# Performance work log

Hardware: AMD Instinct MI355X
Metric: run time of the kernel (lower is better)

## Reference

```python
import jax, jax.numpy as jnp
import numpy as np

B, T, D, F = 4, 1024, 256, 128  # input_dim=D, feature_dim=F, cat_size=1+F


def prelu(x, a):
    # torch.nn.PReLU with a single shared parameter (default init 0.25)
    return jnp.where(x >= 0, x, a * x)


def setup_inputs() -> dict:
    key = jax.random.key(0)
    ks = jax.random.split(key, 10)
    cat = 1 + F
    s1 = 1.0 / np.sqrt(cat)
    s2 = 1.0 / np.sqrt(F)
    return {
        "input": jax.random.normal(ks[0], (B, T, D), jnp.float32),
        "feature": jax.random.normal(ks[1], (B, T, F), jnp.float32),
        "slider": jax.random.uniform(ks[2], (B, T, 1), jnp.float32),
        "W1": jax.random.uniform(ks[3], (F, cat), jnp.float32, -s1, s1),
        "b1": jax.random.uniform(ks[4], (F,), jnp.float32, -s1, s1),
        "a1": jnp.float32(0.25),
        "W2": jax.random.uniform(ks[5], (F, F), jnp.float32, -s2, s2),
        "b2": jax.random.uniform(ks[6], (F,), jnp.float32, -s2, s2),
        "a2": jnp.float32(0.25),
        "Wp": jax.random.uniform(ks[7], (2, cat), jnp.float32, -s1, s1),
        "bp": jax.random.uniform(ks[8], (2,), jnp.float32, -s1, s1),
    }


def reference(input, feature, slider, W1, b1, a1, W2, b2, a2, Wp, bp):
    # input: (B,T,D) -> (B,T,D,1); feature broadcast over D: (B,T,1,F)
    inp = input[..., None]                       # (B,T,D,1)
    feat = feature[..., None, :]                 # (B,T,1,F)
    feat = jnp.broadcast_to(feat, (B, T, D, F))  # repeat across input_dim
    x = jnp.concatenate((inp, feat), axis=-1)    # (B,T,D,1+F)
    # tmlp: Linear -> PReLU -> Linear -> PReLU
    h = prelu(jnp.einsum('btdc,fc->btdf', x, W1) + b1, a1)  # (B,T,D,F)
    h = prelu(jnp.einsum('btdf,gf->btdg', h, W2) + b2, a2)  # (B,T,D,F)
    y = jnp.concatenate((h, inp), axis=-1)       # (B,T,D,1+F)
    p = jnp.einsum('btdc,oc->btdo', y, Wp) + bp  # (B,T,D,2)
    g = p[..., 0:1] * jax.nn.sigmoid(p[..., 1:2])  # GLU(dim=-1) -> (B,T,D,1)
    return (inp * (1.0 + g)).squeeze(-1)         # (B,T,D)
```

## Files before the change

### kernel.cpp

```cpp
#include <hip/hip_runtime.h>
#include <hip/hip_bf16.h>

#define BT 4096
#define DD 256
#define CAT 129

typedef __attribute__((ext_vector_type(8))) __bf16 bf16x8;
typedef __attribute__((ext_vector_type(4))) float f32x4;

static __device__ __forceinline__ unsigned short f2bf(float x) {
    __bf16 b = (__bf16)x;
    return __builtin_bit_cast(unsigned short, b);
}
static __device__ __forceinline__ __bf16 tobf(float x) { return (__bf16)x; }

__global__ void __launch_bounds__(256) k_cvt(
    const float* __restrict__ W1, const float* __restrict__ W2,
    unsigned short* __restrict__ w2bf, unsigned short* __restrict__ w1bf,
    float* __restrict__ w10f)
{
    const int t = threadIdx.x, b = blockIdx.x;
    if (b < 8) {
        #pragma unroll
        for (int i = 0; i < 8; ++i) {
            int idx = b * 2048 + i * 256 + t;
            int g = idx >> 7;
            w2bf[idx ^ ((g & 7) << 3)] = f2bf(W2[idx]);
        }
    } else {
        int q = b - 8;
        #pragma unroll
        for (int i = 0; i < 8; ++i) {
            int idx = q * 2048 + i * 256 + t;
            int f = idx >> 7, c = idx & 127;
            w1bf[idx ^ ((f & 7) << 3)] = f2bf(W1[f * CAT + 1 + c]);
        }
        if (q == 0 && t < 128) w10f[t] = W1[t * CAT];
    }
}

__global__ void __launch_bounds__(256) k_prep2(
    const float* __restrict__ feature, const unsigned short* __restrict__ w1bf,
    const float* __restrict__ b1p, float* __restrict__ v1g)
{
    __shared__ __align__(16) unsigned short fS[2048];
    const int t = threadIdx.x;
    const int r0 = blockIdx.x * 16;

    {
        int e = t * 8;
        int r = e >> 7, c = e & 127;
        const float4* src = (const float4*)(feature + (size_t)(r0 + r) * 128 + c);
        float4 x0 = src[0], x1 = src[1];
        bf16x8 hv;
        hv[0]=tobf(x0.x); hv[1]=tobf(x0.y); hv[2]=tobf(x0.z); hv[3]=tobf(x0.w);
        hv[4]=tobf(x1.x); hv[5]=tobf(x1.y); hv[6]=tobf(x1.z); hv[7]=tobf(x1.w);
        *(bf16x8*)&fS[e ^ ((r & 7) << 3)] = hv;
    }
    __syncthreads();

    const int lane = t & 63, wv = t >> 6;
    const int l15 = lane & 15, l4 = lane >> 4;

    bf16x8 bfr[2][4];
    float4 b1v[2];
    #pragma unroll
    for (int nt = 0; nt < 2; ++nt) {
        const int f0 = wv * 32 + nt * 16;
        b1v[nt] = *(const float4*)(b1p + f0 + l4 * 4);
        #pragma unroll
        for (int kc = 0; kc < 4; ++kc) {
            int f = f0 + l15, c = kc * 32 + l4 * 8;
            bfr[nt][kc] = *(const bf16x8*)&w1bf[(f * 128 + c) ^ ((f & 7) << 3)];
        }
    }

    const f32x4 fz = {0.f, 0.f, 0.f, 0.f};
    f32x4 acc[2] = {fz, fz};
    #pragma unroll
    for (int kc = 0; kc < 4; ++kc) {
        bf16x8 afr;
        {
            int r = l15, c = kc * 32 + l4 * 8;
            afr = *(const bf16x8*)&fS[(r * 128 + c) ^ ((r & 7) << 3)];
        }
        #pragma unroll
        for (int nt = 0; nt < 2; ++nt)
            acc[nt] = __builtin_amdgcn_mfma_f32_16x16x32_bf16(
                bfr[nt][kc], afr, acc[nt], 0, 0, 0);
    }

    #pragma unroll
    for (int nt = 0; nt < 2; ++nt) {
        float4 o;
        o.x = acc[nt][0] + ((const float*)&b1v[nt])[0];
        o.y = acc[nt][1] + ((const float*)&b1v[nt])[1];
        o.z = acc[nt][2] + ((const float*)&b1v[nt])[2];
        o.w = acc[nt][3] + ((const float*)&b1v[nt])[3];
        *(float4*)(v1g + (size_t)(r0 + l15) * 128 + wv * 32 + nt * 16 + l4 * 4) = o;
    }
}

__global__ void __launch_bounds__(512, 4) k_main(
    const float* __restrict__ inp, const float* __restrict__ b2p,
    const float* __restrict__ Wp, const float* __restrict__ bpp,
    const float* __restrict__ a1p, const float* __restrict__ a2p,
    const float* __restrict__ v1g, const unsigned short* __restrict__ w2bf,
    const float* __restrict__ w10f, float* __restrict__ out)
{
    __shared__ __align__(16) unsigned short h1s[8192];
    __shared__ float v1s[8][20];
    __shared__ float w10s[8][20];
    __shared__ float inps[256];
    __shared__ float b2s[128], wpas[128], wpbs[128];
    __shared__ float2 prs[2][4][64];

    const int tid  = threadIdx.x;
    const int lane = tid & 63, wv = tid >> 6;
    const int rg   = wv >> 2, cg = wv & 3;
    const int l15  = lane & 15, l4 = lane >> 4;
    const int bt   = blockIdx.x;

    const float* inpRow = inp + (size_t)bt * DD;
    const float* v1row  = v1g + (size_t)bt * 128;

    if (tid < 256)      inps[tid] = inpRow[tid];
    else if (tid < 384) b2s[tid - 256] = b2p[tid - 256];
    else                wpas[tid - 384] = Wp[tid - 384];
    if (tid < 128)      wpbs[tid] = Wp[CAT + tid];
    else if (tid < 256) { int f = tid - 128; v1s[f >> 4][f & 15]  = v1row[f]; }
    else if (tid < 384) { int f = tid - 256; w10s[f >> 4][f & 15] = w10f[f]; }

    bf16x8 bfr[2][4];
    #pragma unroll
    for (int nt = 0; nt < 2; ++nt) {
        const int g = cg * 32 + nt * 16 + l15;
        #pragma unroll
        for (int kc = 0; kc < 4; ++kc) {
            const int f = kc * 32 + l4 * 8;
            bfr[nt][kc] = *(const bf16x8*)&w2bf[(g * 128 + f) ^ ((g & 7) << 3)];
        }
    }

    const float a1   = a1p[0], a2v = a2p[0];
    const float wpi0 = Wp[128], wpi1 = Wp[CAT + 128];
    const float bp0  = bpp[0],  bp1  = bpp[1];
    __syncthreads();

    const int lr = tid >> 3;
    const int fg = tid & 7;
    const f32x4 fz = {0.f, 0.f, 0.f, 0.f};

    for (int qt = 0; qt < 4; ++qt) {
        float2* prsC = &prs[qt & 1][0][0];

        {
            const float s = inps[qt * 64 + lr];
            #pragma unroll
            for (int f8 = 0; f8 < 2; ++f8) {
                const float4 va0 = *(const float4*)&v1s[fg][f8 * 8];
                const float4 va1 = *(const float4*)&v1s[fg][f8 * 8 + 4];
                const float4 wa0 = *(const float4*)&w10s[fg][f8 * 8];
                const float4 wa1 = *(const float4*)&w10s[fg][f8 * 8 + 4];
                const float va[8] = {va0.x, va0.y, va0.z, va0.w,
                                     va1.x, va1.y, va1.z, va1.w};
                const float wa[8] = {wa0.x, wa0.y, wa0.z, wa0.w,
                                     wa1.x, wa1.y, wa1.z, wa1.w};
                bf16x8 hv;
                #pragma unroll
                for (int j = 0; j < 8; ++j) {
                    float h = fmaf(wa[j], s, va[j]);
                    h = fmaxf(h, 0.f) + a1 * fminf(h, 0.f);
                    hv[j] = (__bf16)h;
                }
                const int idx = (lr * 128 + fg * 16 + f8 * 8) ^ ((lr & 7) << 3);
                *(bf16x8*)&h1s[idx] = hv;
            }
        }
        __syncthreads();

        f32x4 acc[2][2] = {{fz, fz}, {fz, fz}};
        #pragma unroll
        for (int kc = 0; kc < 4; ++kc) {
            bf16x8 afr[2];
            #pragma unroll
            for (int rt = 0; rt < 2; ++rt) {
                const int r = rg * 32 + rt * 16 + l15;
                const int f = kc * 32 + l4 * 8;
                afr[rt] = *(const bf16x8*)&h1s[(r * 128 + f) ^ ((r & 7) << 3)];
            }
            #pragma unroll
            for (int nt = 0; nt < 2; ++nt)
                #pragma unroll
                for (int rt = 0; rt < 2; ++rt)
                    acc[nt][rt] = __builtin_amdgcn_mfma_f32_16x16x32_bf16(
                        bfr[nt][kc], afr[rt], acc[nt][rt], 0, 0, 0);
        }

        float4 b2q[2], wq0[2], wq1[2];
        #pragma unroll
        for (int nt = 0; nt < 2; ++nt) {
            b2q[nt] = *(const float4*)&b2s[cg * 32 + nt * 16 + l4 * 4];
            wq0[nt] = *(const float4*)&wpas[cg * 32 + nt * 16 + l4 * 4];
            wq1[nt] = *(const float4*)&wpbs[cg * 32 + nt * 16 + l4 * 4];
        }
        #pragma unroll
        for (int rt = 0; rt < 2; ++rt) {
            float s0 = 0.f, s1 = 0.f;
            #pragma unroll
            for (int nt = 0; nt < 2; ++nt)
                #pragma unroll
                for (int j = 0; j < 4; ++j) {
                    float h2 = acc[nt][rt][j] + ((const float*)&b2q[nt])[j];
                    h2 = fmaxf(h2, 0.f) + a2v * fminf(h2, 0.f);
                    s0 = fmaf(((const float*)&wq0[nt])[j], h2, s0);
                    s1 = fmaf(((const float*)&wq1[nt])[j], h2, s1);
                }
            s0 += __shfl_xor(s0, 16); s0 += __shfl_xor(s0, 32);
            s1 += __shfl_xor(s1, 16); s1 += __shfl_xor(s1, 32);
            if (l4 == 0) {
                float2 v; v.x = s0; v.y = s1;
                prsC[cg * 64 + rg * 32 + rt * 16 + l15] = v;
            }
        }
        __syncthreads();

        if (wv == 0) {
            const float s = inps[qt * 64 + lane];
            const float2 q0 = prsC[lane],       q1 = prsC[64 + lane];
            const float2 q2 = prsC[128 + lane], q3 = prsC[192 + lane];
            const float e0 = q0.x + q1.x + q2.x + q3.x + wpi0 * s + bp0;
            const float e1 = q0.y + q1.y + q2.y + q3.y + wpi1 * s + bp1;
            const float gg = e0 / (1.f + __expf(-e1));
            out[(size_t)bt * DD + qt * 64 + lane] = s * (1.f + gg);
        }
    }
}

extern "C" void kernel_launch(void* const* d_in, const int* in_sizes, int n_in,
                              void* d_out, int out_size, void* d_ws, size_t ws_size,
                              hipStream_t stream)
{
    (void)in_sizes; (void)n_in; (void)out_size; (void)ws_size;
    const float* input   = (const float*)d_in[0];
    const float* feature = (const float*)d_in[1];
    const float* W1 = (const float*)d_in[3];
    const float* b1 = (const float*)d_in[4];
    const float* a1 = (const float*)d_in[5];
    const float* W2 = (const float*)d_in[6];
    const float* b2 = (const float*)d_in[7];
    const float* a2 = (const float*)d_in[8];
    const float* Wp = (const float*)d_in[9];
    const float* bp = (const float*)d_in[10];
    float* out = (float*)d_out;

    float*          v1g  = (float*)d_ws;
    unsigned short* w2bf = (unsigned short*)((char*)d_ws + (size_t)BT * 128 * 4);
    unsigned short* w1bf = w2bf + 16384;
    float*          w10f = (float*)(w1bf + 16384);

    k_cvt  <<<dim3(16),  dim3(256), 0, stream>>>(W1, W2, w2bf, w1bf, w10f);
    k_prep2<<<dim3(256), dim3(256), 0, stream>>>(feature, w1bf, b1, v1g);
    k_main <<<dim3(BT),  dim3(512), 0, stream>>>(input, b2, Wp, bp, a1, a2,
                                                 v1g, w2bf, w10f, out);
}
```

Measured before the change: 76.97 us.

## Switch to fp16 packed math, two rows per block, pipelined epilogue

Changes bf16 to fp16 throughout and computes the PReLU activations with packed half2 arithmetic and fdot2 for the projection. Each block now handles two (b,t) rows with double-buffered h1 tiles. The GLU epilogue for the previous tile is deferred to one wave after the next barrier, which removes one barrier per tile. W2 is staged through LDS, and b2 is folded into the accumulator initial value. The intent is less VALU and barrier overhead per row, at the cost of fp16 precision and range in the activations.

```diff
diff --git a/kernel.cpp b/kernel.cpp
--- a/kernel.cpp
+++ b/kernel.cpp
@@ -5,19 +5,29 @@
 #define DD 256
 #define CAT 129
 
-typedef __attribute__((ext_vector_type(8))) __bf16 bf16x8;
+typedef __attribute__((ext_vector_type(8))) _Float16 f16x8;
+typedef __attribute__((ext_vector_type(4))) _Float16 f16x4;
+typedef __attribute__((ext_vector_type(2))) _Float16 h2;
 typedef __attribute__((ext_vector_type(4))) float f32x4;
 
-static __device__ __forceinline__ unsigned short f2bf(float x) {
-    __bf16 b = (__bf16)x;
-    return __builtin_bit_cast(unsigned short, b);
-}
-static __device__ __forceinline__ __bf16 tobf(float x) { return (__bf16)x; }
+static __device__ __forceinline__ h2 cvt_pk(float a, float b) {
+    return __builtin_bit_cast(h2, __builtin_amdgcn_cvt_pkrtz(a, b));
+}
+
+static __device__ __forceinline__ float fdot2f(h2 a, h2 b, float c) {
+#if __has_builtin(__builtin_amdgcn_fdot2)
+    return __builtin_amdgcn_fdot2(__builtin_bit_cast(__fp16 __attribute__((ext_vector_type(2))), a),
+                                  __builtin_bit_cast(__fp16 __attribute__((ext_vector_type(2))), b),
+                                  c, false);
+#else
+    return fmaf((float)a[0], (float)b[0], fmaf((float)a[1], (float)b[1], c));
+#endif
+}
 
 __global__ void __launch_bounds__(256) k_cvt(
     const float* __restrict__ W1, const float* __restrict__ W2,
-    unsigned short* __restrict__ w2bf, unsigned short* __restrict__ w1bf,
-    float* __restrict__ w10f)
+    _Float16* __restrict__ w2h, _Float16* __restrict__ w1h,
+    _Float16* __restrict__ w10h)
 {
     const int t = threadIdx.x, b = blockIdx.x;
     if (b < 8) {
@@ -25,7 +35,7 @@
         for (int i = 0; i < 8; ++i) {
             int idx = b * 2048 + i * 256 + t;
             int g = idx >> 7;
-            w2bf[idx ^ ((g & 7) << 3)] = f2bf(W2[idx]);
+            w2h[idx ^ ((g & 7) << 3)] = (_Float16)W2[idx];
         }
     } else {
         int q = b - 8;
@@ -33,17 +43,17 @@
         for (int i = 0; i < 8; ++i) {
             int idx = q * 2048 + i * 256 + t;
             int f = idx >> 7, c = idx & 127;
-            w1bf[idx ^ ((f & 7) << 3)] = f2bf(W1[f * CAT + 1 + c]);
-        }
-        if (q == 0 && t < 128) w10f[t] = W1[t * CAT];
+            w1h[idx ^ ((f & 7) << 3)] = (_Float16)W1[f * CAT + 1 + c];
+        }
+        if (q == 0 && t < 128) w10h[t] = (_Float16)W1[t * CAT];
     }
 }
 
 __global__ void __launch_bounds__(256) k_prep2(
-    const float* __restrict__ feature, const unsigned short* __restrict__ w1bf,
-    const float* __restrict__ b1p, float* __restrict__ v1g)
+    const float* __restrict__ feature, const _Float16* __restrict__ w1h,
+    const float* __restrict__ b1p, _Float16* __restrict__ v1h)
 {
-    __shared__ __align__(16) unsigned short fS[2048];
+    __shared__ __align__(16) _Float16 fS[2048];
     const int t = threadIdx.x;
     const int r0 = blockIdx.x * 16;
 
@@ -52,17 +62,19 @@
         int r = e >> 7, c = e & 127;
         const float4* src = (const float4*)(feature + (size_t)(r0 + r) * 128 + c);
         float4 x0 = src[0], x1 = src[1];
-        bf16x8 hv;
-        hv[0]=tobf(x0.x); hv[1]=tobf(x0.y); hv[2]=tobf(x0.z); hv[3]=tobf(x0.w);
-        hv[4]=tobf(x1.x); hv[5]=tobf(x1.y); hv[6]=tobf(x1.z); hv[7]=tobf(x1.w);
-        *(bf16x8*)&fS[e ^ ((r & 7) << 3)] = hv;
+        f16x8 hv;
+        hv[0] = (_Float16)x0.x; hv[1] = (_Float16)x0.y;
+        hv[2] = (_Float16)x0.z; hv[3] = (_Float16)x0.w;
+        hv[4] = (_Float16)x1.x; hv[5] = (_Float16)x1.y;
+        hv[6] = (_Float16)x1.z; hv[7] = (_Float16)x1.w;
+        *(f16x8*)&fS[e ^ ((r & 7) << 3)] = hv;
     }
     __syncthreads();
 
     const int lane = t & 63, wv = t >> 6;
     const int l15 = lane & 15, l4 = lane >> 4;
 
-    bf16x8 bfr[2][4];
+    f16x8 bfr[2][4];
     float4 b1v[2];
     #pragma unroll
     for (int nt = 0; nt < 2; ++nt) {
@@ -71,7 +83,7 @@
         #pragma unroll
         for (int kc = 0; kc < 4; ++kc) {
             int f = f0 + l15, c = kc * 32 + l4 * 8;
-            bfr[nt][kc] = *(const bf16x8*)&w1bf[(f * 128 + c) ^ ((f & 7) << 3)];
+            bfr[nt][kc] = *(const f16x8*)&w1h[(f * 128 + c) ^ ((f & 7) << 3)];
         }
     }
 
@@ -79,25 +91,22 @@
     f32x4 acc[2] = {fz, fz};
     #pragma unroll
     for (int kc = 0; kc < 4; ++kc) {
-        bf16x8 afr;
-        {
-            int r = l15, c = kc * 32 + l4 * 8;
-            afr = *(const bf16x8*)&fS[(r * 128 + c) ^ ((r & 7) << 3)];
-        }
+        int r = l15, c = kc * 32 + l4 * 8;
+        f16x8 afr = *(const f16x8*)&fS[(r * 128 + c) ^ ((r & 7) << 3)];
         #pragma unroll
         for (int nt = 0; nt < 2; ++nt)
-            acc[nt] = __builtin_amdgcn_mfma_f32_16x16x32_bf16(
+            acc[nt] = __builtin_amdgcn_mfma_f32_16x16x32_f16(
                 bfr[nt][kc], afr, acc[nt], 0, 0, 0);
     }
 
     #pragma unroll
     for (int nt = 0; nt < 2; ++nt) {
-        float4 o;
-        o.x = acc[nt][0] + ((const float*)&b1v[nt])[0];
-        o.y = acc[nt][1] + ((const float*)&b1v[nt])[1];
-        o.z = acc[nt][2] + ((const float*)&b1v[nt])[2];
-        o.w = acc[nt][3] + ((const float*)&b1v[nt])[3];
-        *(float4*)(v1g + (size_t)(r0 + l15) * 128 + wv * 32 + nt * 16 + l4 * 4) = o;
+        f16x4 o;
+        o[0] = (_Float16)(acc[nt][0] + ((const float*)&b1v[nt])[0]);
+        o[1] = (_Float16)(acc[nt][1] + ((const float*)&b1v[nt])[1]);
+        o[2] = (_Float16)(acc[nt][2] + ((const float*)&b1v[nt])[2]);
+        o[3] = (_Float16)(acc[nt][3] + ((const float*)&b1v[nt])[3]);
+        *(f16x4*)&v1h[(size_t)(r0 + l15) * 128 + wv * 32 + nt * 16 + l4 * 4] = o;
     }
 }
 
@@ -105,135 +114,169 @@
     const float* __restrict__ inp, const float* __restrict__ b2p,
     const float* __restrict__ Wp, const float* __restrict__ bpp,
     const float* __restrict__ a1p, const float* __restrict__ a2p,
-    const float* __restrict__ v1g, const unsigned short* __restrict__ w2bf,
-    const float* __restrict__ w10f, float* __restrict__ out)
+    const _Float16* __restrict__ v1h, const _Float16* __restrict__ w2h,
+    const _Float16* __restrict__ w10h, float* __restrict__ out)
 {
-    __shared__ __align__(16) unsigned short h1s[8192];
-    __shared__ float v1s[8][20];
-    __shared__ float w10s[8][20];
-    __shared__ float inps[256];
-    __shared__ float b2s[128], wpas[128], wpbs[128];
+    __shared__ __align__(16) _Float16 h1s[16384];
     __shared__ float2 prs[2][4][64];
+    __shared__ float inps[512];
+    __shared__ _Float16 v1s[256];
+    __shared__ _Float16 w10s[128];
 
     const int tid  = threadIdx.x;
     const int lane = tid & 63, wv = tid >> 6;
     const int rg   = wv >> 2, cg = wv & 3;
     const int l15  = lane & 15, l4 = lane >> 4;
-    const int bt   = blockIdx.x;
-
-    const float* inpRow = inp + (size_t)bt * DD;
-    const float* v1row  = v1g + (size_t)bt * 128;
-
-    if (tid < 256)      inps[tid] = inpRow[tid];
-    else if (tid < 384) b2s[tid - 256] = b2p[tid - 256];
-    else                wpas[tid - 384] = Wp[tid - 384];
-    if (tid < 128)      wpbs[tid] = Wp[CAT + tid];
-    else if (tid < 256) { int f = tid - 128; v1s[f >> 4][f & 15]  = v1row[f]; }
-    else if (tid < 384) { int f = tid - 256; w10s[f >> 4][f & 15] = w10f[f]; }
-
-    bf16x8 bfr[2][4];
+    const int bt0  = blockIdx.x * 2;
+
+    #pragma unroll
+    for (int q = 0; q < 4; ++q)
+        ((int4*)h1s)[q * 512 + tid] = ((const int4*)w2h)[q * 512 + tid];
+    inps[tid] = inp[(size_t)bt0 * DD + tid];
+    if (tid < 128)
+        ((unsigned*)v1s)[tid] = ((const unsigned*)(v1h + (size_t)bt0 * 128))[tid];
+    else if (tid < 192)
+        ((unsigned*)w10s)[tid - 128] = ((const unsigned*)w10h)[tid - 128];
+
+    h2 z2; z2[0] = (_Float16)0.f; z2[1] = (_Float16)0.f;
+    h2 a1v, a2v;
+    { _Float16 x = (_Float16)a1p[0]; a1v[0] = x; a1v[1] = x; }
+    { _Float16 x = (_Float16)a2p[0]; a2v[0] = x; a2v[1] = x; }
+    const float wpi0 = Wp[128], wpi1 = Wp[CAT + 128];
+    const float bp0  = bpp[0],  bp1  = bpp[1];
+
+    f32x4 accInit[2];
+    h2 wpa_pk[2][2], wpb_pk[2][2];
+    #pragma unroll
+    for (int nt = 0; nt < 2; ++nt) {
+        const int g0 = cg * 32 + nt * 16 + l4 * 4;
+        accInit[nt][0] = b2p[g0];     accInit[nt][1] = b2p[g0 + 1];
+        accInit[nt][2] = b2p[g0 + 2]; accInit[nt][3] = b2p[g0 + 3];
+        wpa_pk[nt][0] = cvt_pk(Wp[g0],           Wp[g0 + 1]);
+        wpa_pk[nt][1] = cvt_pk(Wp[g0 + 2],       Wp[g0 + 3]);
+        wpb_pk[nt][0] = cvt_pk(Wp[CAT + g0],     Wp[CAT + g0 + 1]);
+        wpb_pk[nt][1] = cvt_pk(Wp[CAT + g0 + 2], Wp[CAT + g0 + 3]);
+    }
+    __syncthreads();
+
+    f16x8 bfr[2][4];
     #pragma unroll
     for (int nt = 0; nt < 2; ++nt) {
         const int g = cg * 32 + nt * 16 + l15;
         #pragma unroll
+        for (int kc = 0; kc < 4; ++kc)
+            bfr[nt][kc] = *(const f16x8*)
+                &h1s[(g * 128 + kc * 32 + l4 * 8) ^ ((g & 7) << 3)];
+    }
+
+    const int lr = tid >> 3, fg = tid & 7;
+    h2 w10pk[8];
+    #pragma unroll
+    for (int m = 0; m < 8; ++m)
+        w10pk[m] = *(const h2*)&w10s[fg * 16 + m * 2];
+
+    int roff[2][4];
+    #pragma unroll
+    for (int rt = 0; rt < 2; ++rt) {
+        const int R = rg * 32 + rt * 16 + l15;
+        #pragma unroll
+        for (int kc = 0; kc < 4; ++kc)
+            roff[rt][kc] = (R * 128 + kc * 32 + l4 * 8) ^ ((R & 7) << 3);
+    }
+    const int woffA = (lr * 128 + fg * 16)     ^ ((lr & 7) << 3);
+    const int woffB = (lr * 128 + fg * 16 + 8) ^ ((lr & 7) << 3);
+
+    h2 v1pk[8];
+    __syncthreads();
+
+    #pragma unroll 2
+    for (int i = 0; i < 8; ++i) {
+        const int btl = i >> 2, qt = i & 3, buf = i & 1;
+        if (i == 0 || i == 4) {
+            #pragma unroll
+            for (int m = 0; m < 8; ++m)
+                v1pk[m] = *(const h2*)&v1s[btl * 128 + fg * 16 + m * 2];
+        }
+
+        {
+            const float s = inps[btl * 256 + qt * 64 + lr];
+            h2 s2; { _Float16 sh = (_Float16)s; s2[0] = sh; s2[1] = sh; }
+            f16x8 w0, w1;
+            #pragma unroll
+            for (int m = 0; m < 8; ++m) {
+                h2 h  = v1pk[m] + w10pk[m] * s2;
+                h2 hp = __builtin_elementwise_max(h, z2)
+                      + a1v * __builtin_elementwise_min(h, z2);
+                if (m < 4) { w0[2 * m] = hp[0]; w0[2 * m + 1] = hp[1]; }
+                else { w1[2 * (m - 4)] = hp[0]; w1[2 * (m - 4) + 1] = hp[1]; }
+            }
+            *(f16x8*)&h1s[buf * 8192 + woffA] = w0;
+            *(f16x8*)&h1s[buf * 8192 + woffB] = w1;
+        }
+        __syncthreads();
+
+        if (i > 0 && wv == (i - 1)) {
+            const int pb = (i - 1) & 1, pbt = (i - 1) >> 2, pq = (i - 1) & 3;
+            const float s = inps[pbt * 256 + pq * 64 + lane];
+            const float2 t0 = prs[pb][0][lane], t1 = prs[pb][1][lane];
+            const float2 t2 = prs[pb][2][lane], t3 = prs[pb][3][lane];
+            const float e0 = t0.x + t1.x + t2.x + t3.x + wpi0 * s + bp0;
+            const float e1 = t0.y + t1.y + t2.y + t3.y + wpi1 * s + bp1;
+            const float gg = e0 / (1.f + __expf(-e1));
+            out[(size_t)(bt0 + pbt) * DD + pq * 64 + lane] = s * (1.f + gg);
+        }
+
+        f32x4 acc[2][2];
+        #pragma unroll
+        for (int nt = 0; nt < 2; ++nt) {
+            acc[nt][0] = accInit[nt];
+            acc[nt][1] = accInit[nt];
+        }
+        #pragma unroll
         for (int kc = 0; kc < 4; ++kc) {
-            const int f = kc * 32 + l4 * 8;
-            bfr[nt][kc] = *(const bf16x8*)&w2bf[(g * 128 + f) ^ ((g & 7) << 3)];
-        }
-    }
-
-    const float a1   = a1p[0], a2v = a2p[0];
-    const float wpi0 = Wp[128], wpi1 = Wp[CAT + 128];
-    const float bp0  = bpp[0],  bp1  = bpp[1];
-    __syncthreads();
-
-    const int lr = tid >> 3;
-    const int fg = tid & 7;
-    const f32x4 fz = {0.f, 0.f, 0.f, 0.f};
-
-    for (int qt = 0; qt < 4; ++qt) {
-        float2* prsC = &prs[qt & 1][0][0];
-
-        {
-            const float s = inps[qt * 64 + lr];
-            #pragma unroll
-            for (int f8 = 0; f8 < 2; ++f8) {
-                const float4 va0 = *(const float4*)&v1s[fg][f8 * 8];
-                const float4 va1 = *(const float4*)&v1s[fg][f8 * 8 + 4];
-                const float4 wa0 = *(const float4*)&w10s[fg][f8 * 8];
-                const float4 wa1 = *(const float4*)&w10s[fg][f8 * 8 + 4];
-                const float va[8] = {va0.x, va0.y, va0.z, va0.w,
-                                     va1.x, va1.y, va1.z, va1.w};
-                const float wa[8] = {wa0.x, wa0.y, wa0.z, wa0.w,
-                                     wa1.x, wa1.y, wa1.z, wa1.w};
-                bf16x8 hv;
-                #pragma unroll
-                for (int j = 0; j < 8; ++j) {
-                    float h = fmaf(wa[j], s, va[j]);
-                    h = fmaxf(h, 0.f) + a1 * fminf(h, 0.f);
-                    hv[j] = (__bf16)h;
-                }
-                const int idx = (lr * 128 + fg * 16 + f8 * 8) ^ ((lr & 7) << 3);
-                *(bf16x8*)&h1s[idx] = hv;
-            }
-        }
-        __syncthreads();
-
-        f32x4 acc[2][2] = {{fz, fz}, {fz, fz}};
-        #pragma unroll
-        for (int kc = 0; kc < 4; ++kc) {
-            bf16x8 afr[2];
-            #pragma unroll
-            for (int rt = 0; rt < 2; ++rt) {
-                const int r = rg * 32 + rt * 16 + l15;
-                const int f = kc * 32 + l4 * 8;
-                afr[rt] = *(const bf16x8*)&h1s[(r * 128 + f) ^ ((r & 7) << 3)];
-            }
+            f16x8 afr[2];
+            #pragma unroll
+            for (int rt = 0; rt < 2; ++rt)
+                afr[rt] = *(const f16x8*)&h1s[buf * 8192 + roff[rt][kc]];
             #pragma unroll
             for (int nt = 0; nt < 2; ++nt)
                 #pragma unroll
                 for (int rt = 0; rt < 2; ++rt)
-                    acc[nt][rt] = __builtin_amdgcn_mfma_f32_16x16x32_bf16(
+                    acc[nt][rt] = __builtin_amdgcn_mfma_f32_16x16x32_f16(
                         bfr[nt][kc], afr[rt], acc[nt][rt], 0, 0, 0);
         }
 
-        float4 b2q[2], wq0[2], wq1[2];
-        #pragma unroll
-        for (int nt = 0; nt < 2; ++nt) {
-            b2q[nt] = *(const float4*)&b2s[cg * 32 + nt * 16 + l4 * 4];
-            wq0[nt] = *(const float4*)&wpas[cg * 32 + nt * 16 + l4 * 4];
-            wq1[nt] = *(const float4*)&wpbs[cg * 32 + nt * 16 + l4 * 4];
-        }
         #pragma unroll
         for (int rt = 0; rt < 2; ++rt) {
             float s0 = 0.f, s1 = 0.f;
             #pragma unroll
             for (int nt = 0; nt < 2; ++nt)
                 #pragma unroll
-                for (int j = 0; j < 4; ++j) {
-                    float h2 = acc[nt][rt][j] + ((const float*)&b2q[nt])[j];
-                    h2 = fmaxf(h2, 0.f) + a2v * fminf(h2, 0.f);
-                    s0 = fmaf(((const float*)&wq0[nt])[j], h2, s0);
-                    s1 = fmaf(((const float*)&wq1[nt])[j], h2, s1);
+                for (int p = 0; p < 2; ++p) {
+                    h2 hh = cvt_pk(acc[nt][rt][2 * p], acc[nt][rt][2 * p + 1]);
+                    h2 hp = __builtin_elementwise_max(hh, z2)
+                          + a2v * __builtin_elementwise_min(hh, z2);
+                    s0 = fdot2f(wpa_pk[nt][p], hp, s0);
+                    s1 = fdot2f(wpb_pk[nt][p], hp, s1);
                 }
             s0 += __shfl_xor(s0, 16); s0 += __shfl_xor(s0, 32);
             s1 += __shfl_xor(s1, 16); s1 += __shfl_xor(s1, 32);
             if (l4 == 0) {
                 float2 v; v.x = s0; v.y = s1;
-                prsC[cg * 64 + rg * 32 + rt * 16 + l15] = v;
+                prs[buf][cg][rg * 32 + rt * 16 + l15] = v;
             }
         }
-        __syncthreads();
-
-        if (wv == 0) {
-            const float s = inps[qt * 64 + lane];
-            const float2 q0 = prsC[lane],       q1 = prsC[64 + lane];
-            const float2 q2 = prsC[128 + lane], q3 = prsC[192 + lane];
-            const float e0 = q0.x + q1.x + q2.x + q3.x + wpi0 * s + bp0;
-            const float e1 = q0.y + q1.y + q2.y + q3.y + wpi1 * s + bp1;
-            const float gg = e0 / (1.f + __expf(-e1));
-            out[(size_t)bt * DD + qt * 64 + lane] = s * (1.f + gg);
-        }
+    }
+
+    __syncthreads();
+    if (wv == 7) {
+        const float s = inps[256 + 192 + lane];
+        const float2 t0 = prs[1][0][lane], t1 = prs[1][1][lane];
+        const float2 t2 = prs[1][2][lane], t3 = prs[1][3][lane];
+        const float e0 = t0.x + t1.x + t2.x + t3.x + wpi0 * s + bp0;
+        const float e1 = t0.y + t1.y + t2.y + t3.y + wpi1 * s + bp1;
+        const float gg = e0 / (1.f + __expf(-e1));
+        out[(size_t)(bt0 + 1) * DD + 192 + lane] = s * (1.f + gg);
     }
 }
 
@@ -254,13 +297,13 @@
     const float* bp = (const float*)d_in[10];
     float* out = (float*)d_out;
 
-    float*          v1g  = (float*)d_ws;
-    unsigned short* w2bf = (unsigned short*)((char*)d_ws + (size_t)BT * 128 * 4);
-    unsigned short* w1bf = w2bf + 16384;
-    float*          w10f = (float*)(w1bf + 16384);
-
-    k_cvt  <<<dim3(16),  dim3(256), 0, stream>>>(W1, W2, w2bf, w1bf, w10f);
-    k_prep2<<<dim3(256), dim3(256), 0, stream>>>(feature, w1bf, b1, v1g);
-    k_main <<<dim3(BT),  dim3(512), 0, stream>>>(input, b2, Wp, bp, a1, a2,
-                                                 v1g, w2bf, w10f, out);
-}
+    _Float16* v1h  = (_Float16*)d_ws;
+    _Float16* w2h  = v1h + (size_t)BT * 128;
+    _Float16* w1h  = w2h + 16384;
+    _Float16* w10h = w1h + 16384;
+
+    k_cvt  <<<dim3(16),   dim3(256), 0, stream>>>(W1, W2, w2h, w1h, w10h);
+    k_prep2<<<dim3(256),  dim3(256), 0, stream>>>(feature, w1h, b1, v1h);
+    k_main <<<dim3(2048), dim3(512), 0, stream>>>(input, b2, Wp, bp, a1, a2,
+                                                  v1h, w2h, w10h, out);
+}
```

New measurement: 63.76 us. 17.2% less time.
